# Kernel optimization log

Hardware: AMD Instinct MI355X
Metric: run time of the kernel (lower is better)

Reference implementation:

```python
import jax, jax.numpy as jnp
import numpy as np

D_MODEL = 512
NUM_HEADS = 8
HEAD_DIM = D_MODEL // NUM_HEADS
MAX_REL = 2


def setup_inputs() -> dict:
    key = jax.random.key(0)
    ks = jax.random.split(key, 12)
    B, S = 2, 4096
    std = 1.0 / np.sqrt(D_MODEL)
    inp = {
        'q': jax.random.normal(ks[0], (B, S, D_MODEL), jnp.float32),
        'k': jax.random.normal(ks[1], (B, S, D_MODEL), jnp.float32),
        'v': jax.random.normal(ks[2], (B, S, D_MODEL), jnp.float32),
        'Wq': jax.random.normal(ks[3], (D_MODEL, D_MODEL), jnp.float32) * std,
        'bq': jnp.zeros((D_MODEL,), jnp.float32),
        'Wk': jax.random.normal(ks[4], (D_MODEL, D_MODEL), jnp.float32) * std,
        'bk': jnp.zeros((D_MODEL,), jnp.float32),
        'Wv': jax.random.normal(ks[5], (D_MODEL, D_MODEL), jnp.float32) * std,
        'bv': jnp.zeros((D_MODEL,), jnp.float32),
        'Wo': jax.random.normal(ks[6], (D_MODEL, D_MODEL), jnp.float32) * std,
        'bo': jnp.zeros((D_MODEL,), jnp.float32),
        'rel_pos': jax.random.normal(ks[7], (NUM_HEADS, 2 * MAX_REL + 1), jnp.float32),
    }
    return inp


def _rel_bias(rel_pos, seq_len):
    pos = jnp.arange(seq_len)
    rel = pos[None, :] - pos[:, None]              # [S,S]
    idx = jnp.clip(rel, -MAX_REL, MAX_REL) + MAX_REL
    return rel_pos[:, idx]                         # [H,S,S]


def reference(q, k, v, Wq, bq, Wk, bk, Wv, bv, Wo, bo, rel_pos):
    B, S, D = q.shape
    H, Hd = NUM_HEADS, HEAD_DIM
    # torch Linear: x @ W.T + b
    Q = (q @ Wq.T + bq).reshape(B, S, H, Hd).transpose(0, 2, 1, 3)  # [B,H,S,Hd]
    K = (k @ Wk.T + bk).reshape(B, S, H, Hd).transpose(0, 2, 1, 3)
    V = (v @ Wv.T + bv).reshape(B, S, H, Hd).transpose(0, 2, 1, 3)
    scores = jnp.einsum('bhqd,bhkd->bhqk', Q, K) / jnp.sqrt(jnp.float32(Hd))
    scores = scores + _rel_bias(rel_pos, S)[None]                  # [B,H,S,S]
    probs = jax.nn.softmax(scores, axis=-1)
    attn = jnp.einsum('bhqk,bhkd->bhqd', probs, V)                 # [B,H,S,Hd]
    attn = attn.transpose(0, 2, 1, 3).reshape(B, S, D)
    return attn @ Wo.T + bo
```

## Files before the change

kernel.cpp:

```cpp
#include <hip/hip_runtime.h>

typedef __bf16 bf16_t;
typedef __bf16 bf16x2 __attribute__((ext_vector_type(2)));
typedef __bf16 bf16x4 __attribute__((ext_vector_type(4)));
typedef __bf16 bf16x8 __attribute__((ext_vector_type(8)));
typedef float f32x4 __attribute__((ext_vector_type(4)));
typedef unsigned int u32x4 __attribute__((ext_vector_type(4)));

#define MFMA16(a, b, c) __builtin_amdgcn_mfma_f32_16x16x32_bf16(a, b, c, 0, 0, 0)
#define LOG2E 1.4426950408889634f
#define SHIFT 16.0f

#define GLL(g, l)                                                      \
  __builtin_amdgcn_global_load_lds(                                    \
      (const __attribute__((address_space(1))) void*)(g),              \
      (__attribute__((address_space(3))) void*)(l), 16, 0, 0)

#define WAIT_BARRIER_V4() asm volatile("s_waitcnt vmcnt(4)\n\ts_barrier" ::: "memory")
#define WAIT_BARRIER_V6() asm volatile("s_waitcnt vmcnt(6)\n\ts_barrier" ::: "memory")
#define WAIT_BARRIER_V8() asm volatile("s_waitcnt vmcnt(8)\n\ts_barrier" ::: "memory")

static constexpr int NB = 2;
static constexpr int SEQ = 4096;
static constexpr int DM = 512;
static constexpr int NH = 8;
static constexpr int HD = 64;
static constexpr int M_ROWS = NB * SEQ;

__global__ __launch_bounds__(256) void cvt_w_kernel(
    const float* __restrict__ w0, const float* __restrict__ w1,
    const float* __restrict__ w2, const float* __restrict__ w3,
    bf16_t* __restrict__ out) {
  const float* src = (blockIdx.y == 0) ? w0 : (blockIdx.y == 1) ? w1
                   : (blockIdx.y == 2) ? w2 : w3;
  int i = (blockIdx.x * 256 + threadIdx.x) * 4;
  float4 v = *(const float4*)(src + i);
  bf16_t* o = out + blockIdx.y * (DM * DM) + i;
  o[0] = (bf16_t)v.x; o[1] = (bf16_t)v.y; o[2] = (bf16_t)v.z; o[3] = (bf16_t)v.w;
}

__global__ __launch_bounds__(256) void cvt_x_kernel(
    const float* __restrict__ q, const float* __restrict__ k,
    const float* __restrict__ v, bf16_t* __restrict__ out) {
  const float* src = (blockIdx.y == 0) ? q : (blockIdx.y == 1) ? k : v;
  bf16_t* dst = out + (size_t)blockIdx.y * (M_ROWS * DM);
  int i = (blockIdx.x * 256 + threadIdx.x) * 8;
  float4 a = *(const float4*)(src + i);
  float4 b = *(const float4*)(src + i + 4);
  bf16x8 o;
  o[0] = (bf16_t)a.x; o[1] = (bf16_t)a.y; o[2] = (bf16_t)a.z; o[3] = (bf16_t)a.w;
  o[4] = (bf16_t)b.x; o[5] = (bf16_t)b.y; o[6] = (bf16_t)b.z; o[7] = (bf16_t)b.w;
  *(bf16x8*)(dst + i) = o;
}

__device__ __forceinline__ void gemm_body64(
    const bf16_t* __restrict__ X, const bf16_t* __restrict__ Wm,
    const float* __restrict__ bias, void* __restrict__ Out,
    int omode, float scale) {
  __shared__ bf16_t Asm[3][64 * 64];
  __shared__ bf16_t Bsm[3][128 * 64];

  const int tid = threadIdx.x;
  const int w = tid >> 6;
  const int lane = tid & 63;
  const int quad = lane >> 4, l15 = lane & 15;
  const int l8 = lane >> 3;
  const int swcol = ((lane & 7) ^ l8) * 8;
  const int m0 = blockIdx.x * 64;
  const int n0 = blockIdx.y * 128;
  const int moff = (w & 1) * 32;
  const int noff = (w >> 1) * 64;

  f32x4 acc[2][4];
#pragma unroll
  for (int mb = 0; mb < 2; mb++)
#pragma unroll
    for (int nb = 0; nb < 4; nb++) { acc[mb][nb][0] = 0.f; acc[mb][nb][1] = 0.f; acc[mb][nb][2] = 0.f; acc[mb][nb][3] = 0.f; }

  auto stage = [&](int ks, int bufi) {
    const int k0 = ks * 64;
#pragma unroll
    for (int j = 0; j < 4; j++) {
      const int row = j * 32 + w * 8 + l8;
      GLL(Wm + (size_t)(n0 + row) * DM + k0 + swcol, &Bsm[bufi][(j * 256 + w * 64) * 8]);
    }
#pragma unroll
    for (int j = 0; j < 2; j++) {
      const int row = j * 32 + w * 8 + l8;
      GLL(X + (size_t)(m0 + row) * DM + k0 + swcol, &Asm[bufi][(j * 256 + w * 64) * 8]);
    }
  };

  stage(0, 0);
  stage(1, 1);

  for (int ks = 0; ks < 8; ks++) {
    WAIT_BARRIER_V6();
    const int tn = (ks + 2 < 8) ? ks + 2 : 7;
    stage(tn, (ks + 2) % 3);
    const int p = ks % 3;

#pragma unroll
    for (int kd = 0; kd < 2; kd++) {
      const int fch = (((kd << 2) + quad) ^ (l15 & 7)) << 3;
      bf16x8 bfr[4];
#pragma unroll
      for (int nb = 0; nb < 4; nb++)
        bfr[nb] = *(const bf16x8*)&Bsm[p][(noff + nb * 16 + l15) * 64 + fch];
#pragma unroll
      for (int mb = 0; mb < 2; mb++) {
        bf16x8 a = *(const bf16x8*)&Asm[p][(moff + mb * 16 + l15) * 64 + fch];
#pragma unroll
        for (int nb = 0; nb < 4; nb++) acc[mb][nb] = MFMA16(a, bfr[nb], acc[mb][nb]);
      }
    }
  }

#pragma unroll
  for (int nb = 0; nb < 4; nb++) {
    const int n = n0 + noff + nb * 16 + l15;
    const float bn = bias[n];
    const int h = n >> 6, dd = n & 63;
#pragma unroll
    for (int mb = 0; mb < 2; mb++) {
      const int mbase = m0 + moff + mb * 16 + quad * 4;
      const int bb = mbase >> 12, s = mbase & 4095;
      if (omode == 0) {
#pragma unroll
        for (int r = 0; r < 4; r++) {
          const float val = (acc[mb][nb][r] + bn) * scale;
          ((bf16_t*)Out)[(size_t)((bb * NH + h) * SEQ + s + r) * HD + dd] = (bf16_t)val;
        }
      } else if (omode == 1) {
        bf16x4 pk;
#pragma unroll
        for (int r = 0; r < 4; r++) pk[r] = (bf16_t)(acc[mb][nb][r] + bn);
        *(bf16x4*)&((bf16_t*)Out)[(((size_t)(bb * NH + h) * HD + dd) << 12) + s] = pk;
      } else {
#pragma unroll
        for (int r = 0; r < 4; r++)
          ((float*)Out)[(size_t)(mbase + r) * DM + n] = acc[mb][nb][r] + bn;
      }
    }
  }
}

__global__ __launch_bounds__(256, 2) void qkv_kernel(
    const bf16_t* __restrict__ Xall, const bf16_t* __restrict__ Wall,
    const float* __restrict__ bq, const float* __restrict__ bk,
    const float* __restrict__ bv, bf16_t* __restrict__ Qb,
    bf16_t* __restrict__ Kb, bf16_t* __restrict__ Vb, float qscale) {
  const int z = blockIdx.z;
  const bf16_t* X = Xall + (size_t)z * (M_ROWS * DM);
  const float* bias = (z == 0) ? bq : (z == 1) ? bk : bv;
  bf16_t* Out = (z == 0) ? Qb : (z == 1) ? Kb : Vb;
  gemm_body64(X, Wall + (size_t)z * DM * DM, bias, Out,
              (z == 2) ? 1 : 0, (z == 0) ? qscale : 1.0f);
}

__global__ __launch_bounds__(256, 2) void oproj_kernel(
    const bf16_t* __restrict__ X, const bf16_t* __restrict__ Wm,
    const float* __restrict__ bias, float* __restrict__ Out) {
  gemm_body64(X, Wm, bias, Out, 2, 1.0f);
}

__global__ __launch_bounds__(256, 2) void attn_kernel(
    const bf16_t* __restrict__ Qb, const bf16_t* __restrict__ Kb,
    const bf16_t* __restrict__ Vb, const float* __restrict__ rel_pos,
    bf16_t* __restrict__ attn_out) {
  __shared__ bf16_t Kt[4][64 * 64];
  __shared__ bf16_t Vt[4][64 * 64];

  const int tid = threadIdx.x;
  const int w = tid >> 6;
  const int lane = tid & 63;
  const int quad = lane >> 4, l15 = lane & 15;
  const int wq = w >> 1, wk = w & 1;

  const int lin = blockIdx.x;
  const int glob = (lin & 7) * 64 + (lin >> 3);
  const int bh = glob >> 5;
  const int qb = glob & 31;
  const int b = bh >> 3, h = bh & 7;
  const int qlo = qb * 128 + wq * 64;

  const float rb0 = rel_pos[h * 5 + 0] * LOG2E;
  const float rb1 = rel_pos[h * 5 + 1] * LOG2E;
  const float rb2 = rel_pos[h * 5 + 2] * LOG2E;
  const float rb3 = rel_pos[h * 5 + 3] * LOG2E;
  const float rb4 = rel_pos[h * 5 + 4] * LOG2E;

  bf16x8 qf[4][2];
#pragma unroll
  for (int mb = 0; mb < 4; mb++)
#pragma unroll
    for (int kd = 0; kd < 2; kd++)
      qf[mb][kd] = *(const bf16x8*)(Qb + (size_t)(bh * SEQ + qlo + mb * 16 + l15) * HD + kd * 32 + 8 * quad);

  f32x4 o[4][4];
#pragma unroll
  for (int mb = 0; mb < 4; mb++)
#pragma unroll
    for (int db = 0; db < 4; db++) { o[mb][db][0] = 0.f; o[mb][db][1] = 0.f; o[mb][db][2] = 0.f; o[mb][db][3] = 0.f; }
  f32x4 l4[4];
#pragma unroll
  for (int mb = 0; mb < 4; mb++) { l4[mb][0] = 0.f; l4[mb][1] = 0.f; l4[mb][2] = 0.f; l4[mb][3] = 0.f; }

  bf16x8 ones;
#pragma unroll
  for (int i = 0; i < 8; i++) ones[i] = (bf16_t)1.0f;

  const int srow = (w << 4) + (lane >> 3);
  const int scol = (((lane & 7) ^ (lane >> 3)) << 3);
  const bf16_t* kg0 = Kb + ((size_t)(bh * SEQ + srow) << 6) + scol;
  const bf16_t* vg0 = Vb + (((size_t)(bh * HD + srow)) << 12) + scol;
  const int ldst = (w << 10);

  const int sw = l15 & 7;
  const int kfo0 = (l15 << 6) + ((quad ^ sw) << 3);
  const int kfo1 = (l15 << 6) + (((quad + 4) ^ sw) << 3);
  const int vfo = (l15 << 6) + ((((wk << 2) + quad) ^ sw) << 3);
  const int wk2 = wk << 1;

  auto stage = [&](int t, int bufi) {
    GLL(kg0 + ((size_t)t << 12), &Kt[bufi][ldst]);
    GLL(kg0 + ((size_t)t << 12) + (8 << 6), &Kt[bufi][ldst + 512]);
    GLL(vg0 + (t << 6), &Vt[bufi][ldst]);
    GLL(vg0 + (t << 6) + (8 << 12), &Vt[bufi][ldst + 512]);
  };

  auto qk_tile = [&](int tq, f32x4 (&s)[4][2]) {
    const int klo = tq * 64 + wk * 32;
    float cini;
    if (klo >= qlo + 65)        cini = rb4 - SHIFT;
    else if (klo <= qlo - 33)   cini = rb0 - SHIFT;
    else                        cini = -SHIFT;
#pragma unroll
    for (int mb = 0; mb < 4; mb++)
#pragma unroll
      for (int kb = 0; kb < 2; kb++) { s[mb][kb][0] = cini; s[mb][kb][1] = cini; s[mb][kb][2] = cini; s[mb][kb][3] = cini; }
    const int pq = tq & 3;
    __builtin_amdgcn_s_setprio(1);
#pragma unroll
    for (int kb = 0; kb < 2; kb++) {
      bf16x8 kA0 = *(const bf16x8*)&Kt[pq][kfo0 + ((wk2 + kb) << 10)];
      bf16x8 kA1 = *(const bf16x8*)&Kt[pq][kfo1 + ((wk2 + kb) << 10)];
      s[0][kb] = MFMA16(kA0, qf[0][0], s[0][kb]);
      s[0][kb] = MFMA16(kA1, qf[0][1], s[0][kb]);
      s[1][kb] = MFMA16(kA0, qf[1][0], s[1][kb]);
      s[1][kb] = MFMA16(kA1, qf[1][1], s[1][kb]);
      s[2][kb] = MFMA16(kA0, qf[2][0], s[2][kb]);
      s[2][kb] = MFMA16(kA1, qf[2][1], s[2][kb]);
      s[3][kb] = MFMA16(kA0, qf[3][0], s[3][kb]);
      s[3][kb] = MFMA16(kA1, qf[3][1], s[3][kb]);
    }
    __builtin_amdgcn_s_setprio(0);
  };

  auto sm_pv = [&](int t, f32x4 (&s)[4][2]) {
    const int klo = t * 64 + wk * 32;
    const bool nearband = !(klo >= qlo + 65) && !(klo <= qlo - 33);
    if (nearband) {
#pragma unroll
      for (int mb = 0; mb < 4; mb++) {
        const int qg = qlo + mb * 16 + l15;
#pragma unroll
        for (int kb = 0; kb < 2; kb++)
#pragma unroll
          for (int r = 0; r < 4; r++) {
            int dl = klo + kb * 16 + quad * 4 + r - qg;
            float bias = dl <= -2 ? rb0
                       : (dl >= 2 ? rb4
                       : (dl == -1 ? rb1 : (dl == 0 ? rb2 : rb3)));
            s[mb][kb][r] += bias;
          }
      }
    }

    bf16x8 pf[4];
#pragma unroll
    for (int mb = 0; mb < 4; mb++) {
      unsigned int u[2][2];
#pragma unroll
      for (int kb = 0; kb < 2; kb++) {
        bf16x2 p0, p1;
        p0[0] = (bf16_t)__builtin_amdgcn_exp2f(s[mb][kb][0]);
        p0[1] = (bf16_t)__builtin_amdgcn_exp2f(s[mb][kb][1]);
        p1[0] = (bf16_t)__builtin_amdgcn_exp2f(s[mb][kb][2]);
        p1[1] = (bf16_t)__builtin_amdgcn_exp2f(s[mb][kb][3]);
        u[kb][0] = __builtin_bit_cast(unsigned int, p0);
        u[kb][1] = __builtin_bit_cast(unsigned int, p1);
      }
      unsigned int a0 = u[0][0], b0 = u[1][0];
      unsigned int a1 = u[0][1], b1 = u[1][1];
      asm("v_permlane32_swap_b32 %0, %1" : "+v"(a0), "+v"(b0));
      asm("v_permlane32_swap_b32 %0, %1" : "+v"(a1), "+v"(b1));
      asm("v_permlane16_swap_b32 %0, %1" : "+v"(a0), "+v"(b0));
      asm("v_permlane16_swap_b32 %0, %1" : "+v"(a1), "+v"(b1));
      u32x4 pk; pk[0] = a0; pk[1] = a1; pk[2] = b0; pk[3] = b1;
      pf[mb] = __builtin_bit_cast(bf16x8, pk);
    }

    const int p = t & 3;
    __builtin_amdgcn_s_setprio(1);
    l4[0] = MFMA16(ones, pf[0], l4[0]);
    l4[1] = MFMA16(ones, pf[1], l4[1]);
    l4[2] = MFMA16(ones, pf[2], l4[2]);
    l4[3] = MFMA16(ones, pf[3], l4[3]);
#pragma unroll
    for (int db = 0; db < 4; db++) {
      bf16x8 vA = *(const bf16x8*)&Vt[p][vfo + (db << 10)];
      o[0][db] = MFMA16(vA, pf[0], o[0][db]);
      o[1][db] = MFMA16(vA, pf[1], o[1][db]);
      o[2][db] = MFMA16(vA, pf[2], o[2][db]);
      o[3][db] = MFMA16(vA, pf[3], o[3][db]);
    }
    __builtin_amdgcn_s_setprio(0);
  };

  stage(0, 0);
  stage(1, 1);
  stage(2, 2);
  WAIT_BARRIER_V8();

  f32x4 sA[4][2], sB[4][2];
  qk_tile(0, sA);

  for (int t2 = 0; t2 < 32; t2++) {
    {
      const int t = 2 * t2;
      WAIT_BARRIER_V4();
      const int tg = (t + 3 < 64) ? t + 3 : 63;
      stage(tg, (t + 3) & 3);
      qk_tile(t + 1, sB);
      sm_pv(t, sA);
    }
    {
      const int t = 2 * t2 + 1;
      WAIT_BARRIER_V4();
      const int tg = (t + 3 < 64) ? t + 3 : 63;
      stage(tg, (t + 3) & 3);
      if (t < 63) qk_tile(t + 1, sA);
      sm_pv(t, sB);
    }
  }

  asm volatile("s_waitcnt vmcnt(0)" ::: "memory");
  __syncthreads();
  float* Ored = (float*)&Kt[0][0];
  float* lred = (float*)&Vt[0][0];
  if (wk) {
#pragma unroll
    for (int mb = 0; mb < 4; mb++) {
      lred[(wq << 6) + (mb << 4) + l15] = l4[mb][0];
#pragma unroll
      for (int db = 0; db < 4; db++) {
        const int ch = ((db << 2) | quad) ^ sw;
        *(f32x4*)&Ored[(wq << 12) + ((mb * 16 + l15) << 6) + (ch << 2)] = o[mb][db];
      }
    }
  }
  __syncthreads();
  if (!wk) {
#pragma unroll
    for (int mb = 0; mb < 4; mb++) {
      float lsum = l4[mb][0] + lred[(wq << 6) + (mb << 4) + l15];
      const float inv = 1.0f / lsum;
      const int qg = qlo + mb * 16 + l15;
#pragma unroll
      for (int db = 0; db < 4; db++) {
        const int ch = ((db << 2) | quad) ^ sw;
        const f32x4 part = *(const f32x4*)&Ored[(wq << 12) + ((mb * 16 + l15) << 6) + (ch << 2)];
        bf16x4 pk;
#pragma unroll
        for (int r = 0; r < 4; r++) pk[r] = (bf16_t)((o[mb][db][r] + part[r]) * inv);
        *(bf16x4*)(attn_out + (size_t)(b * SEQ + qg) * DM + h * HD + db * 16 + quad * 4) = pk;
      }
    }
  }
}

extern "C" void kernel_launch(void* const* d_in, const int* in_sizes, int n_in,
                              void* d_out, int out_size, void* d_ws, size_t ws_size,
                              hipStream_t stream) {
  const float* q   = (const float*)d_in[0];
  const float* k   = (const float*)d_in[1];
  const float* v   = (const float*)d_in[2];
  const float* Wq  = (const float*)d_in[3];
  const float* bq  = (const float*)d_in[4];
  const float* Wk  = (const float*)d_in[5];
  const float* bk  = (const float*)d_in[6];
  const float* Wv  = (const float*)d_in[7];
  const float* bv  = (const float*)d_in[8];
  const float* Wo  = (const float*)d_in[9];
  const float* bo  = (const float*)d_in[10];
  const float* rel = (const float*)d_in[11];

  char* ws = (char*)d_ws;
  bf16_t* Wbf  = (bf16_t*)ws;
  bf16_t* Xb   = (bf16_t*)(ws + (size_t)(2  << 20));
  bf16_t* Qbuf = (bf16_t*)(ws + (size_t)(26 << 20));
  bf16_t* Kbuf = (bf16_t*)(ws + (size_t)(34 << 20));
  bf16_t* Vbuf = (bf16_t*)(ws + (size_t)(42 << 20));
  bf16_t* Abuf = (bf16_t*)(ws + (size_t)(2  << 20));

  cvt_w_kernel<<<dim3(256, 4), 256, 0, stream>>>(Wq, Wk, Wv, Wo, Wbf);
  cvt_x_kernel<<<dim3(2048, 3), 256, 0, stream>>>(q, k, v, Xb);

  const float qscale = LOG2E / 8.0f;
  qkv_kernel<<<dim3(128, 4, 3), 256, 0, stream>>>(
      Xb, Wbf, bq, bk, bv, Qbuf, Kbuf, Vbuf, qscale);

  attn_kernel<<<512, 256, 0, stream>>>(Qbuf, Kbuf, Vbuf, rel, Abuf);

  oproj_kernel<<<dim3(128, 4), 256, 0, stream>>>(Abuf, Wbf + 3 * DM * DM, bo, (float*)d_out);
}
```

Measured before the change: 230.8 us.

## Restructure attention main loop to process tile pairs with one barrier per pair

The software pipeline changes from staging one K/V tile three ahead per iteration, with a vmcnt(4) barrier and QK of the next tile overlapped with softmax·V of the current one, to one loop over pairs of tiles. Each pair waits for all loads (vmcnt(0)), stages the next two tiles, runs QK for both tiles and then softmax·V for both. This halves the barrier count and groups MFMA work. The cost is a shorter prefetch distance and a full drain of outstanding loads at every barrier, which may expose memory latency.

```diff
diff --git a/kernel.cpp b/kernel.cpp
--- a/kernel.cpp
+++ b/kernel.cpp
@@ -16,9 +16,8 @@
       (const __attribute__((address_space(1))) void*)(g),              \
       (__attribute__((address_space(3))) void*)(l), 16, 0, 0)
 
-#define WAIT_BARRIER_V4() asm volatile("s_waitcnt vmcnt(4)\n\ts_barrier" ::: "memory")
+#define WAIT_BARRIER_V0() asm volatile("s_waitcnt vmcnt(0)\n\ts_barrier" ::: "memory")
 #define WAIT_BARRIER_V6() asm volatile("s_waitcnt vmcnt(6)\n\ts_barrier" ::: "memory")
-#define WAIT_BARRIER_V8() asm volatile("s_waitcnt vmcnt(8)\n\ts_barrier" ::: "memory")
 
 static constexpr int NB = 2;
 static constexpr int SEQ = 4096;
@@ -320,29 +319,20 @@
 
   stage(0, 0);
   stage(1, 1);
-  stage(2, 2);
-  WAIT_BARRIER_V8();
 
   f32x4 sA[4][2], sB[4][2];
-  qk_tile(0, sA);
-
-  for (int t2 = 0; t2 < 32; t2++) {
-    {
-      const int t = 2 * t2;
-      WAIT_BARRIER_V4();
-      const int tg = (t + 3 < 64) ? t + 3 : 63;
-      stage(tg, (t + 3) & 3);
-      qk_tile(t + 1, sB);
-      sm_pv(t, sA);
-    }
-    {
-      const int t = 2 * t2 + 1;
-      WAIT_BARRIER_V4();
-      const int tg = (t + 3 < 64) ? t + 3 : 63;
-      stage(tg, (t + 3) & 3);
-      if (t < 63) qk_tile(t + 1, sA);
-      sm_pv(t, sB);
-    }
+
+  for (int j = 0; j < 32; j++) {
+    const int e = 2 * j, o2 = 2 * j + 1;
+    WAIT_BARRIER_V0();
+    const int ta = (e + 2 < 64) ? e + 2 : 63;
+    const int tb = (o2 + 2 < 64) ? o2 + 2 : 63;
+    stage(ta, (e + 2) & 3);
+    stage(tb, (o2 + 2) & 3);
+    qk_tile(e, sA);
+    qk_tile(o2, sB);
+    sm_pv(e, sA);
+    sm_pv(o2, sB);
   }
 
   asm volatile("s_waitcnt vmcnt(0)" ::: "memory");
```

Result: no change. 227.2 us (-1.6%).
